# Optimization experiments

Measured on AMD Instinct MI355X. Metric: run time of the kernel, lower is better.

The kernel has to match this reference:

```python
import jax, jax.numpy as jnp
import numpy as np
import math

B, S, D, H = 2, 2048, 1024, 16
DK = D // H  # 64

def setup_inputs() -> dict:
    key = jax.random.key(0)
    ks = jax.random.split(key, 12)
    scale = 1.0 / math.sqrt(D)
    inp = {
        "query": jax.random.normal(ks[0], (B, S, D), jnp.float32),
        "key_": jax.random.normal(ks[1], (B, S, D), jnp.float32),
        "value": jax.random.normal(ks[2], (B, S, D), jnp.float32),
        "mask": jax.random.randint(ks[3], (B, 1, S, S), 0, 2, jnp.int32),
        "Wq": jax.random.normal(ks[4], (D, D), jnp.float32) * scale,
        "bq": jnp.zeros((D,), jnp.float32),
        "Wk": jax.random.normal(ks[5], (D, D), jnp.float32) * scale,
        "bk": jnp.zeros((D,), jnp.float32),
        "Wv": jax.random.normal(ks[6], (D, D), jnp.float32) * scale,
        "bv": jnp.zeros((D,), jnp.float32),
        "Wo": jax.random.normal(ks[7], (D, D), jnp.float32) * scale,
        "bo": jnp.zeros((D,), jnp.float32),
    }
    return inp

def _split_heads(x):  # [B,S,D] -> [B,H,S,DK]
    return x.reshape(B, -1, H, DK).transpose(0, 2, 1, 3)

def reference(query, key_, value, mask, Wq, bq, Wk, bk, Wv, bv, Wo, bo):
    # torch nn.Linear: y = x @ W^T + b
    q = _split_heads(query @ Wq.T + bq)
    k = _split_heads(key_ @ Wk.T + bk)
    v = _split_heads(value @ Wv.T + bv)
    scores = jnp.einsum("bhqd,bhkd->bhqk", q, k) / math.sqrt(DK)
    scores = jnp.where(mask == 0, jnp.float32(-1e9), scores)
    attn = jax.nn.softmax(scores, axis=-1)  # dropout is identity in eval mode
    ctx = jnp.einsum("bhqk,bhkd->bhqd", attn, v)
    ctx = ctx.transpose(0, 2, 1, 3).reshape(B, -1, D)
    return ctx @ Wo.T + bo
```

## Files before the change

kernel.cpp:

```cpp
#include <hip/hip_runtime.h>
#include <hip/hip_bf16.h>

typedef short s16x8 __attribute__((ext_vector_type(8)));
typedef float f32x4 __attribute__((ext_vector_type(4)));
typedef unsigned short u16;
typedef unsigned int u32;
typedef unsigned long long u64;

__device__ __forceinline__ u16 f2bf(float f) {
    union { float f; unsigned u; } c; c.f = f;
    unsigned u = c.u;
    return (u16)((u + 0x7fffu + ((u >> 16) & 1u)) >> 16);
}
__device__ __forceinline__ float bf2f(u32 lo16) {
    union { unsigned u; float f; } c; c.u = lo16 << 16; return c.f;
}
__device__ __forceinline__ u32 cvtpk(float lo, float hi) {
    u32 r;
    asm("v_cvt_pk_bf16_f32 %0, %1, %2" : "=v"(r) : "v"(lo), "v"(hi));
    return r;
}
__device__ __forceinline__ void gload16(const void* g, void* l) {
    __builtin_amdgcn_global_load_lds(
        (const __attribute__((address_space(1))) void*)g,
        (__attribute__((address_space(3))) void*)l, 16, 0, 0);
}

__global__ __launch_bounds__(256)
void conv_k(const float* __restrict__ q, const float* __restrict__ k, const float* __restrict__ v,
            const float* __restrict__ wq, const float* __restrict__ wk, const float* __restrict__ wv,
            const float* __restrict__ wo,
            u16* __restrict__ Qf, u16* __restrict__ Kf, u16* __restrict__ Vf,
            u16* __restrict__ Wqb, u16* __restrict__ Wkb, u16* __restrict__ Wvb, u16* __restrict__ Wob)
{
    const int gi = blockIdx.x * 256 + threadIdx.x;
    const float* src; u16* dst; int base;
    if (gi < 3 * 1048576) {
        const int seg = gi / 1048576;
        base = (gi - seg * 1048576) * 4;
        src = seg == 0 ? q : seg == 1 ? k : v;
        dst = seg == 0 ? Qf : seg == 1 ? Kf : Vf;
    } else {
        const int g2 = gi - 3 * 1048576;
        const int seg = g2 / 262144;
        base = (g2 - seg * 262144) * 4;
        src = seg == 0 ? wq : seg == 1 ? wk : seg == 2 ? wv : wo;
        dst = seg == 0 ? Wqb : seg == 1 ? Wkb : seg == 2 ? Wvb : Wob;
    }
    const float4 x = *(const float4*)(src + base);
    uint2 pk;
    pk.x = f2bf(x.x) | ((unsigned)f2bf(x.y) << 16);
    pk.y = f2bf(x.z) | ((unsigned)f2bf(x.w) << 16);
    *(uint2*)(dst + base) = pk;
}

__global__ __launch_bounds__(256)
void qkv_k(const u16* __restrict__ A0, const u16* __restrict__ A1, const u16* __restrict__ A2,
           const u16* __restrict__ W0, const u16* __restrict__ W1, const u16* __restrict__ W2,
           const float* __restrict__ b0, const float* __restrict__ b1, const float* __restrict__ b2,
           u16* __restrict__ O0, u16* __restrict__ O1, u16* __restrict__ O2)
{
    __shared__ u16 As[128 * 32];
    __shared__ u16 Bs[128 * 32];
    const int z = blockIdx.z;
    const u16* A = z == 0 ? A0 : z == 1 ? A1 : A2;
    const u16* W = z == 0 ? W0 : z == 1 ? W1 : W2;
    const float* bias = z == 0 ? b0 : z == 1 ? b1 : b2;
    u16* O = z == 0 ? O0 : z == 1 ? O1 : O2;

    const int tid = threadIdx.x, lane = tid & 63, wave = tid >> 6;
    const int wm = wave >> 1, wn = wave & 1;
    const int g = lane >> 4, q15 = lane & 15;
    const int m0 = blockIdx.x * 128, n0 = blockIdx.y * 128;
    const int lrow = lane >> 2, lcol = (lane & 3) * 8;

    f32x4 acc[4][4];
    #pragma unroll
    for (int i = 0; i < 4; i++)
        #pragma unroll
        for (int j = 0; j < 4; j++) acc[i][j] = f32x4{0.f, 0.f, 0.f, 0.f};

    for (int k0 = 0; k0 < 1024; k0 += 32) {
        __syncthreads();
        #pragma unroll
        for (int i = 0; i < 2; i++) {
            const int rr = i * 64 + wave * 16 + lrow;
            gload16(A + (size_t)(m0 + rr) * 1024 + k0 + lcol, &As[(i * 64 + wave * 16) * 32]);
            gload16(W + (size_t)(n0 + rr) * 1024 + k0 + lcol, &Bs[(i * 64 + wave * 16) * 32]);
        }
        __syncthreads();

        s16x8 af[4], bfr[4];
        #pragma unroll
        for (int mi = 0; mi < 4; mi++) af[mi]  = *(const s16x8*)&As[(wm * 64 + mi * 16 + q15) * 32 + g * 8];
        #pragma unroll
        for (int ni = 0; ni < 4; ni++) bfr[ni] = *(const s16x8*)&Bs[(wn * 64 + ni * 16 + q15) * 32 + g * 8];
        #pragma unroll
        for (int mi = 0; mi < 4; mi++)
            #pragma unroll
            for (int ni = 0; ni < 4; ni++)
                acc[mi][ni] = __builtin_amdgcn_mfma_f32_16x16x32_bf16(af[mi], bfr[ni], acc[mi][ni], 0, 0, 0);
    }

    #pragma unroll
    for (int mi = 0; mi < 4; mi++) {
        #pragma unroll
        for (int ni = 0; ni < 4; ni++) {
            const int n = n0 + wn * 64 + ni * 16 + q15;
            const float bn = bias[n];
            const int mbase = m0 + wm * 64 + mi * 16 + g * 4;
            if (z < 2) {
                #pragma unroll
                for (int r = 0; r < 4; r++)
                    O[(size_t)(mbase + r) * 1024 + n] = f2bf(acc[mi][ni][r] + bn);
            } else {
                const int bb = mbase >> 11;
                const int s  = mbase & 2047;
                const int h  = n >> 6, d = n & 63;
                u16 hv[4];
                #pragma unroll
                for (int r = 0; r < 4; r++) hv[r] = f2bf(acc[mi][ni][r] + bn);
                uint2 pk;
                pk.x = hv[0] | ((unsigned)hv[1] << 16);
                pk.y = hv[2] | ((unsigned)hv[3] << 16);
                *(uint2*)&O[(((size_t)(bb * 16 + h) * 64 + d) << 11) + s] = pk;
            }
        }
    }
}

__global__ __launch_bounds__(256)
void og_k(const u16* __restrict__ A, const u16* __restrict__ W,
          const float* __restrict__ bias, float* __restrict__ C)
{
    __shared__ u16 As[64 * 32];
    __shared__ u16 Bs[128 * 32];
    const int tid = threadIdx.x, lane = tid & 63, wave = tid >> 6;
    const int wm = wave >> 1, wn = wave & 1;
    const int g = lane >> 4, q15 = lane & 15;
    const int m0 = blockIdx.x * 64, n0 = blockIdx.y * 128;
    const int lrow = lane >> 2, lcol = (lane & 3) * 8;

    f32x4 acc[2][4];
    #pragma unroll
    for (int i = 0; i < 2; i++)
        #pragma unroll
        for (int j = 0; j < 4; j++) acc[i][j] = f32x4{0.f, 0.f, 0.f, 0.f};

    for (int k0 = 0; k0 < 1024; k0 += 32) {
        __syncthreads();
        {
            const int rr = wave * 16 + lrow;
            gload16(A + (size_t)(m0 + rr) * 1024 + k0 + lcol, &As[(wave * 16) * 32]);
        }
        #pragma unroll
        for (int i = 0; i < 2; i++) {
            const int rr = i * 64 + wave * 16 + lrow;
            gload16(W + (size_t)(n0 + rr) * 1024 + k0 + lcol, &Bs[(i * 64 + wave * 16) * 32]);
        }
        __syncthreads();

        s16x8 af[2], bfr[4];
        #pragma unroll
        for (int mi = 0; mi < 2; mi++) af[mi]  = *(const s16x8*)&As[(wm * 32 + mi * 16 + q15) * 32 + g * 8];
        #pragma unroll
        for (int ni = 0; ni < 4; ni++) bfr[ni] = *(const s16x8*)&Bs[(wn * 64 + ni * 16 + q15) * 32 + g * 8];
        #pragma unroll
        for (int mi = 0; mi < 2; mi++)
            #pragma unroll
            for (int ni = 0; ni < 4; ni++)
                acc[mi][ni] = __builtin_amdgcn_mfma_f32_16x16x32_bf16(af[mi], bfr[ni], acc[mi][ni], 0, 0, 0);
    }

    #pragma unroll
    for (int mi = 0; mi < 2; mi++) {
        #pragma unroll
        for (int ni = 0; ni < 4; ni++) {
            const int n = n0 + wn * 64 + ni * 16 + q15;
            const float bn = bias[n];
            const int mbase = m0 + wm * 32 + mi * 16 + g * 4;
            #pragma unroll
            for (int r = 0; r < 4; r++)
                C[(size_t)(mbase + r) * 1024 + n] = acc[mi][ni][r] + bn;
        }
    }
}

__global__ __launch_bounds__(256)
void pack_mask_k(const int* __restrict__ mask, u64* __restrict__ MB)
{
    const int wid  = blockIdx.x * 4 + (threadIdx.x >> 6);
    const int lane = threadIdx.x & 63;
    const int v = mask[(size_t)wid * 64 + lane];
    const u64 bits = __ballot(v != 0);
    if (lane == 0) MB[wid] = bits;
}

__global__ __launch_bounds__(256, 4)
void attn_k(const u16* __restrict__ Q, const u16* __restrict__ K,
            const u16* __restrict__ Vt, const u64* __restrict__ MB,
            u16* __restrict__ CtxP, float* __restrict__ LsumP)
{
    constexpr int S = 2048, D = 1024, DK = 64;
    __shared__ u16 Ks[64][72];
    __shared__ u16 Vs[64][72];
    __shared__ u16 Ps[4][32][72];
    const int tid = threadIdx.x, lane = tid & 63, wave = tid >> 6;
    const int g = lane >> 4, q15 = lane & 15;
    const int h = blockIdx.y;
    const int b = blockIdx.z >> 1, half = blockIdx.z & 1;
    const int qw = blockIdx.x * 128 + wave * 32;

    s16x8 qf[2][2];
    #pragma unroll
    for (int mf = 0; mf < 2; mf++)
        #pragma unroll
        for (int cc = 0; cc < 2; cc++)
            qf[mf][cc] = *(const s16x8*)(Q + ((size_t)b * S + qw + mf * 16 + q15) * D
                                           + h * DK + cc * 32 + g * 8);

    f32x4 accv[2][4];
    #pragma unroll
    for (int mf = 0; mf < 2; mf++)
        #pragma unroll
        for (int nf = 0; nf < 4; nf++)
            accv[mf][nf] = f32x4{0.f, 0.f, 0.f, 0.f};
    float lsum[2] = {0.f, 0.f};

    const size_t kgbase = (size_t)b * S * D + h * DK;
    const size_t vgbase = ((size_t)b * 16 + h) * DK * S;
    const size_t mbase  = ((size_t)b * S + qw + q15) * 32;

    for (int t = half * 16; t < half * 16 + 16; t++) {
        const int kv0 = t * 64;
        const u64 mw0 = MB[mbase + t];
        const u64 mw1 = MB[mbase + 512 + t];

        __syncthreads();
        #pragma unroll
        for (int i = 0; i < 2; i++) {
            const int c = tid + i * 256;
            const int row = c >> 3, col8 = (c & 7) * 8;
            *(s16x8*)&Ks[row][col8] = *(const s16x8*)(K + kgbase + (size_t)(kv0 + row) * D + col8);
            *(s16x8*)&Vs[row][col8] = *(const s16x8*)(Vt + vgbase + (size_t)row * S + kv0 + col8);
        }
        __syncthreads();

        f32x4 sc[2][4];
        #pragma unroll
        for (int nf = 0; nf < 4; nf++) {
            const s16x8 ka0 = *(const s16x8*)&Ks[nf * 16 + q15][g * 8];
            const s16x8 ka1 = *(const s16x8*)&Ks[nf * 16 + q15][32 + g * 8];
            #pragma unroll
            for (int mf = 0; mf < 2; mf++) {
                f32x4 s = f32x4{0.f, 0.f, 0.f, 0.f};
                s = __builtin_amdgcn_mfma_f32_16x16x32_bf16(ka0, qf[mf][0], s, 0, 0, 0);
                s = __builtin_amdgcn_mfma_f32_16x16x32_bf16(ka1, qf[mf][1], s, 0, 0, 0);
                sc[mf][nf] = s;
            }
        }

        #pragma unroll
        for (int mf = 0; mf < 2; mf++) {
            const u64 mw = mf ? mw1 : mw0;
            float part = 0.f;
            #pragma unroll
            for (int nf = 0; nf < 4; nf++) {
                const u32 nib = (u32)(mw >> (nf * 16 + g * 4)) & 0xFu;
                float p[4];
                #pragma unroll
                for (int r = 0; r < 4; r++) {
                    const float e = __expf(fmaf(sc[mf][nf][r], 0.125f, -8.0f));
                    p[r] = ((nib >> r) & 1u) ? e : 0.f;
                }
                part += (p[0] + p[1]) + (p[2] + p[3]);
                uint2 pk2;
                pk2.x = cvtpk(p[0], p[1]);
                pk2.y = cvtpk(p[2], p[3]);
                *(uint2*)&Ps[wave][mf * 16 + q15][nf * 16 + g * 4] = pk2;
            }
            lsum[mf] += part;
        }

        #pragma unroll
        for (int cc = 0; cc < 2; cc++) {
            s16x8 pa[2];
            #pragma unroll
            for (int mf = 0; mf < 2; mf++)
                pa[mf] = *(const s16x8*)&Ps[wave][mf * 16 + q15][cc * 32 + g * 8];
            #pragma unroll
            for (int nf = 0; nf < 4; nf++) {
                const s16x8 vb = *(const s16x8*)&Vs[nf * 16 + q15][cc * 32 + g * 8];
                #pragma unroll
                for (int mf = 0; mf < 2; mf++)
                    accv[mf][nf] = __builtin_amdgcn_mfma_f32_16x16x32_bf16(pa[mf], vb, accv[mf][nf], 0, 0, 0);
            }
        }
    }

    #pragma unroll
    for (int mf = 0; mf < 2; mf++) {
        float s_ = lsum[mf];
        s_ += __shfl_xor(s_, 16, 64);
        s_ += __shfl_xor(s_, 32, 64);
        lsum[mf] = s_;
    }
    const size_t pbase = (size_t)((half * 2 + b) * 16 + h) * S;
    if (lane < 16) {
        LsumP[pbase + qw + q15]      = lsum[0];
        LsumP[pbase + qw + 16 + q15] = lsum[1];
    }
    #pragma unroll
    for (int mf = 0; mf < 2; mf++)
        #pragma unroll
        for (int nf = 0; nf < 4; nf++)
            #pragma unroll
            for (int r = 0; r < 4; r++) {
                const int qrow = qw + mf * 16 + g * 4 + r;
                CtxP[(pbase + qrow) * 64 + nf * 16 + q15] = f2bf(accv[mf][nf][r]);
            }
}

__global__ __launch_bounds__(256)
void comb_k(const u16* __restrict__ CtxP, const float* __restrict__ LsumP,
            u16* __restrict__ Cx)
{
    const int gid = blockIdx.x * 256 + threadIdx.x;
    const int d4 = gid & 15;
    const int q  = (gid >> 4) & 2047;
    const int h  = (gid >> 15) & 15;
    const int bb = gid >> 19;
    const size_t i0 = ((size_t)(bb * 16 + h)) * 2048 + q;
    const size_t i1 = ((size_t)((2 + bb) * 16 + h)) * 2048 + q;
    const uint2 a = *(const uint2*)&CtxP[i0 * 64 + d4 * 4];
    const uint2 c = *(const uint2*)&CtxP[i1 * 64 + d4 * 4];
    const float rinv = __builtin_amdgcn_rcpf(LsumP[i0] + LsumP[i1]);
    const u32 au[2] = {a.x, a.y}, cu[2] = {c.x, c.y};
    uint2 o;
    u32 ow[2];
    #pragma unroll
    for (int j = 0; j < 2; j++) {
        const float lo = (bf2f(au[j] & 0xffffu) + bf2f(cu[j] & 0xffffu)) * rinv;
        const float hi = (bf2f(au[j] >> 16)     + bf2f(cu[j] >> 16))     * rinv;
        ow[j] = f2bf(lo) | ((u32)f2bf(hi) << 16);
    }
    o.x = ow[0]; o.y = ow[1];
    *(uint2*)&Cx[((size_t)bb * 2048 + q) * 1024 + h * 64 + d4 * 4] = o;
}

extern "C" void kernel_launch(void* const* d_in, const int* in_sizes, int n_in,
                              void* d_out, int out_size, void* d_ws, size_t ws_size,
                              hipStream_t stream)
{
    const float* query = (const float*)d_in[0];
    const float* key_  = (const float*)d_in[1];
    const float* value = (const float*)d_in[2];
    const int*   mask  = (const int*)d_in[3];
    const float* Wq = (const float*)d_in[4];
    const float* bq = (const float*)d_in[5];
    const float* Wk = (const float*)d_in[6];
    const float* bk = (const float*)d_in[7];
    const float* Wv = (const float*)d_in[8];
    const float* bv = (const float*)d_in[9];
    const float* Wo = (const float*)d_in[10];
    const float* bo = (const float*)d_in[11];

    char* ws = (char*)d_ws;
    u16* Qf   = (u16*)(ws);
    u16* Kf   = (u16*)(ws + (size_t)( 8 << 20));
    u16* Vf   = (u16*)(ws + (size_t)(16 << 20));
    u16* Wqb  = (u16*)(ws + (size_t)(24 << 20));
    u16* Wkb  = (u16*)(ws + (size_t)(26 << 20));
    u16* Wvb  = (u16*)(ws + (size_t)(28 << 20));
    u16* Wob  = (u16*)(ws + (size_t)(30 << 20));
    u16* Qb   = (u16*)(ws + (size_t)(32 << 20));
    u16* Kb   = (u16*)(ws + (size_t)(40 << 20));
    u16* Vt   = (u16*)(ws + (size_t)(48 << 20));
    u64* MBp  = (u64*)(ws + (size_t)(56 << 20));
    float* LsP = (float*)(ws + (size_t)(57 << 20));
    u16* CtxP = Qf;
    u16* Cx   = Qb;

    dim3 bb2(256, 1, 1);
    conv_k<<<dim3(16384, 1, 1), bb2, 0, stream>>>(query, key_, value, Wq, Wk, Wv, Wo,
                                                  Qf, Kf, Vf, Wqb, Wkb, Wvb, Wob);
    qkv_k<<<dim3(32, 8, 3), bb2, 0, stream>>>(Qf, Kf, Vf, Wqb, Wkb, Wvb,
                                              bq, bk, bv, Qb, Kb, Vt);
    pack_mask_k<<<dim3(32768, 1, 1), bb2, 0, stream>>>(mask, MBp);
    attn_k<<<dim3(16, 16, 4), bb2, 0, stream>>>(Qb, Kb, Vt, MBp, CtxP, LsP);
    comb_k<<<dim3(4096, 1, 1), bb2, 0, stream>>>(CtxP, LsP, Cx);
    og_k<<<dim3(64, 8, 1), bb2, 0, stream>>>(Cx, Wob, bo, (float*)d_out);
}
```

Before: 173.7 us.

## Rewrite attention kernel with 32x32 MFMA, register-resident P, and double-buffered async staging

Reworks the attention inner loop to use 32x32x16 bf16 MFMAs. The S^T layout lets the exponentiated probabilities feed the PV MFMA straight from registers, which removes the per-wave LDS round trip for P. K/V tiles are staged with global_load_lds into XOR-swizzled double buffers, so the next tile's load overlaps compute, with explicit vmcnt waits and barriers. The exp is switched to exp2 with a folded scale, and setprio hints are added around the MFMA blocks. This increases register pressure and adds complex swizzle indexing that must match the MFMA operand layouts.

```diff
diff --git a/kernel.cpp b/kernel.cpp
--- a/kernel.cpp
+++ b/kernel.cpp
@@ -2,7 +2,9 @@
 #include <hip/hip_bf16.h>
 
 typedef short s16x8 __attribute__((ext_vector_type(8)));
+typedef short s16x4 __attribute__((ext_vector_type(4)));
 typedef float f32x4 __attribute__((ext_vector_type(4)));
+typedef float f32x16 __attribute__((ext_vector_type(16)));
 typedef unsigned short u16;
 typedef unsigned int u32;
 typedef unsigned long long u64;
@@ -116,14 +118,14 @@
             } else {
                 const int bb = mbase >> 11;
                 const int s  = mbase & 2047;
-                const int h  = n >> 6, d = n & 63;
+                const int hd = n >> 6, d = n & 63;
                 u16 hv[4];
                 #pragma unroll
                 for (int r = 0; r < 4; r++) hv[r] = f2bf(acc[mi][ni][r] + bn);
                 uint2 pk;
                 pk.x = hv[0] | ((unsigned)hv[1] << 16);
                 pk.y = hv[2] | ((unsigned)hv[3] << 16);
-                *(uint2*)&O[(((size_t)(bb * 16 + h) * 64 + d) << 11) + s] = pk;
+                *(uint2*)&O[(((size_t)(bb * 16 + hd) * 64 + d) << 11) + s] = pk;
             }
         }
     }
@@ -201,124 +203,124 @@
             const u16* __restrict__ Vt, const u64* __restrict__ MB,
             u16* __restrict__ CtxP, float* __restrict__ LsumP)
 {
-    constexpr int S = 2048, D = 1024, DK = 64;
-    __shared__ u16 Ks[64][72];
-    __shared__ u16 Vs[64][72];
-    __shared__ u16 Ps[4][32][72];
+    constexpr int S = 2048;
+    __shared__ u16 Ks[2][64][64];
+    __shared__ u16 Vs[2][64][64];
     const int tid = threadIdx.x, lane = tid & 63, wave = tid >> 6;
-    const int g = lane >> 4, q15 = lane & 15;
-    const int h = blockIdx.y;
+    const int l31 = lane & 31, h = lane >> 5, x7 = lane & 7;
+    const int hh = blockIdx.y;
     const int b = blockIdx.z >> 1, half = blockIdx.z & 1;
     const int qw = blockIdx.x * 128 + wave * 32;
-
-    s16x8 qf[2][2];
-    #pragma unroll
-    for (int mf = 0; mf < 2; mf++)
-        #pragma unroll
-        for (int cc = 0; cc < 2; cc++)
-            qf[mf][cc] = *(const s16x8*)(Q + ((size_t)b * S + qw + mf * 16 + q15) * D
-                                           + h * DK + cc * 32 + g * 8);
-
-    f32x4 accv[2][4];
-    #pragma unroll
-    for (int mf = 0; mf < 2; mf++)
-        #pragma unroll
-        for (int nf = 0; nf < 4; nf++)
-            accv[mf][nf] = f32x4{0.f, 0.f, 0.f, 0.f};
-    float lsum[2] = {0.f, 0.f};
-
-    const size_t kgbase = (size_t)b * S * D + h * DK;
-    const size_t vgbase = ((size_t)b * 16 + h) * DK * S;
-    const size_t mbase  = ((size_t)b * S + qw + q15) * 32;
-
-    for (int t = half * 16; t < half * 16 + 16; t++) {
-        const int kv0 = t * 64;
-        const u64 mw0 = MB[mbase + t];
-        const u64 mw1 = MB[mbase + 512 + t];
-
-        __syncthreads();
+    const int t0 = half * 16;
+
+    const size_t kgbase = (size_t)b * S * 1024 + hh * 64;
+    const size_t vgbase = (size_t)(b * 16 + hh) * 64 * 2048;
+
+    s16x8 qf[4];
+    #pragma unroll
+    for (int s = 0; s < 4; s++)
+        qf[s] = *(const s16x8*)(Q + ((size_t)b * S + qw + l31) * 1024 + hh * 64 + s * 16 + h * 8);
+
+    f32x16 acc[2];
+    #pragma unroll
+    for (int r = 0; r < 16; r++) { acc[0][r] = 0.f; acc[1][r] = 0.f; }
+    float lsum = 0.f;
+
+    const int srl = lane >> 3;
+    const int scs = ((lane & 7) ^ srl) * 8;
+    auto STAGE = [&](int buf, int kv0) {
         #pragma unroll
         for (int i = 0; i < 2; i++) {
-            const int c = tid + i * 256;
-            const int row = c >> 3, col8 = (c & 7) * 8;
-            *(s16x8*)&Ks[row][col8] = *(const s16x8*)(K + kgbase + (size_t)(kv0 + row) * D + col8);
-            *(s16x8*)&Vs[row][col8] = *(const s16x8*)(Vt + vgbase + (size_t)row * S + kv0 + col8);
-        }
-        __syncthreads();
-
-        f32x4 sc[2][4];
-        #pragma unroll
-        for (int nf = 0; nf < 4; nf++) {
-            const s16x8 ka0 = *(const s16x8*)&Ks[nf * 16 + q15][g * 8];
-            const s16x8 ka1 = *(const s16x8*)&Ks[nf * 16 + q15][32 + g * 8];
-            #pragma unroll
-            for (int mf = 0; mf < 2; mf++) {
-                f32x4 s = f32x4{0.f, 0.f, 0.f, 0.f};
-                s = __builtin_amdgcn_mfma_f32_16x16x32_bf16(ka0, qf[mf][0], s, 0, 0, 0);
-                s = __builtin_amdgcn_mfma_f32_16x16x32_bf16(ka1, qf[mf][1], s, 0, 0, 0);
-                sc[mf][nf] = s;
+            const int rb = i * 32 + wave * 8;
+            gload16(K + kgbase + (size_t)(kv0 + rb + srl) * 1024 + scs, &Ks[buf][rb][0]);
+            gload16(Vt + vgbase + (size_t)(rb + srl) * 2048 + kv0 + scs, &Vs[buf][rb][0]);
+        }
+    };
+
+    const u64* mwp = MB + ((size_t)b * S + qw + l31) * 32 + t0;
+    STAGE(0, t0 * 64);
+
+    for (int t = 0; t < 16; t++) {
+        const int buf = t & 1;
+        const u64 mw = mwp[t];
+        if (t < 15) {
+            STAGE(buf ^ 1, (t0 + t + 1) * 64);
+            asm volatile("s_waitcnt vmcnt(4)" ::: "memory");
+        } else {
+            asm volatile("s_waitcnt vmcnt(0)" ::: "memory");
+        }
+        __builtin_amdgcn_s_barrier();
+        __builtin_amdgcn_sched_barrier(0);
+
+        f32x16 sc[2];
+        #pragma unroll
+        for (int r = 0; r < 16; r++) { sc[0][r] = 0.f; sc[1][r] = 0.f; }
+        __builtin_amdgcn_s_setprio(1);
+        #pragma unroll
+        for (int s = 0; s < 4; s++) {
+            const int ce = (((s << 1) | h) ^ x7) << 3;
+            const s16x8 ka0 = *(const s16x8*)&Ks[buf][l31][ce];
+            const s16x8 ka1 = *(const s16x8*)&Ks[buf][32 + l31][ce];
+            sc[0] = __builtin_amdgcn_mfma_f32_32x32x16_bf16(ka0, qf[s], sc[0], 0, 0, 0);
+            sc[1] = __builtin_amdgcn_mfma_f32_32x32x16_bf16(ka1, qf[s], sc[1], 0, 0, 0);
+        }
+        __builtin_amdgcn_s_setprio(0);
+
+        s16x8 pa[4];
+        #pragma unroll
+        for (int kvb = 0; kvb < 2; kvb++) {
+            const u32 mh = ((u32)(mw >> (kvb * 32))) >> (h * 4);
+            float p[16];
+            #pragma unroll
+            for (int r = 0; r < 16; r++) {
+                const int bit = (r & 3) + ((r >> 2) << 3);
+                const float e = __builtin_amdgcn_exp2f(fmaf(sc[kvb][r], 0.18033688f, -11.5415603f));
+                p[r] = ((mh >> bit) & 1u) ? e : 0.f;
             }
-        }
-
-        #pragma unroll
-        for (int mf = 0; mf < 2; mf++) {
-            const u64 mw = mf ? mw1 : mw0;
-            float part = 0.f;
-            #pragma unroll
-            for (int nf = 0; nf < 4; nf++) {
-                const u32 nib = (u32)(mw >> (nf * 16 + g * 4)) & 0xFu;
-                float p[4];
-                #pragma unroll
-                for (int r = 0; r < 4; r++) {
-                    const float e = __expf(fmaf(sc[mf][nf][r], 0.125f, -8.0f));
-                    p[r] = ((nib >> r) & 1u) ? e : 0.f;
-                }
-                part += (p[0] + p[1]) + (p[2] + p[3]);
-                uint2 pk2;
-                pk2.x = cvtpk(p[0], p[1]);
-                pk2.y = cvtpk(p[2], p[3]);
-                *(uint2*)&Ps[wave][mf * 16 + q15][nf * 16 + g * 4] = pk2;
+            lsum += (((p[0] + p[1]) + (p[2] + p[3])) + ((p[4] + p[5]) + (p[6] + p[7])))
+                  + (((p[8] + p[9]) + (p[10] + p[11])) + ((p[12] + p[13]) + (p[14] + p[15])));
+            #pragma unroll
+            for (int sub = 0; sub < 2; sub++) {
+                const int base = sub * 8;
+                union { u32 w[4]; s16x8 v; } u;
+                u.w[0] = cvtpk(p[base + 0], p[base + 1]);
+                u.w[1] = cvtpk(p[base + 2], p[base + 3]);
+                u.w[2] = cvtpk(p[base + 4], p[base + 5]);
+                u.w[3] = cvtpk(p[base + 6], p[base + 7]);
+                pa[kvb * 2 + sub] = u.v;
             }
-            lsum[mf] += part;
-        }
-
-        #pragma unroll
-        for (int cc = 0; cc < 2; cc++) {
-            s16x8 pa[2];
-            #pragma unroll
-            for (int mf = 0; mf < 2; mf++)
-                pa[mf] = *(const s16x8*)&Ps[wave][mf * 16 + q15][cc * 32 + g * 8];
-            #pragma unroll
-            for (int nf = 0; nf < 4; nf++) {
-                const s16x8 vb = *(const s16x8*)&Vs[nf * 16 + q15][cc * 32 + g * 8];
-                #pragma unroll
-                for (int mf = 0; mf < 2; mf++)
-                    accv[mf][nf] = __builtin_amdgcn_mfma_f32_16x16x32_bf16(pa[mf], vb, accv[mf][nf], 0, 0, 0);
-            }
-        }
-    }
-
-    #pragma unroll
-    for (int mf = 0; mf < 2; mf++) {
-        float s_ = lsum[mf];
-        s_ += __shfl_xor(s_, 16, 64);
-        s_ += __shfl_xor(s_, 32, 64);
-        lsum[mf] = s_;
-    }
-    const size_t pbase = (size_t)((half * 2 + b) * 16 + h) * S;
-    if (lane < 16) {
-        LsumP[pbase + qw + q15]      = lsum[0];
-        LsumP[pbase + qw + 16 + q15] = lsum[1];
-    }
-    #pragma unroll
-    for (int mf = 0; mf < 2; mf++)
-        #pragma unroll
-        for (int nf = 0; nf < 4; nf++)
-            #pragma unroll
-            for (int r = 0; r < 4; r++) {
-                const int qrow = qw + mf * 16 + g * 4 + r;
-                CtxP[(pbase + qrow) * 64 + nf * 16 + q15] = f2bf(accv[mf][nf][r]);
-            }
+        }
+
+        __builtin_amdgcn_s_setprio(1);
+        #pragma unroll
+        for (int s = 0; s < 4; s++) {
+            const int e0 = (((2 * s)     ^ x7) << 3) + 4 * h;
+            const int e1 = (((2 * s + 1) ^ x7) << 3) + 4 * h;
+            union { s16x4 q2[2]; s16x8 v; } u0, u1;
+            u0.q2[0] = *(const s16x4*)&Vs[buf][l31][e0];
+            u0.q2[1] = *(const s16x4*)&Vs[buf][l31][e1];
+            u1.q2[0] = *(const s16x4*)&Vs[buf][32 + l31][e0];
+            u1.q2[1] = *(const s16x4*)&Vs[buf][32 + l31][e1];
+            acc[0] = __builtin_amdgcn_mfma_f32_32x32x16_bf16(pa[s], u0.v, acc[0], 0, 0, 0);
+            acc[1] = __builtin_amdgcn_mfma_f32_32x32x16_bf16(pa[s], u1.v, acc[1], 0, 0, 0);
+        }
+        __builtin_amdgcn_s_setprio(0);
+        __builtin_amdgcn_s_barrier();
+    }
+
+    lsum += __shfl_xor(lsum, 32, 64);
+    const size_t pbase = (size_t)((half * 2 + b) * 16 + hh) * S;
+    if (lane < 32) LsumP[pbase + qw + l31] = lsum;
+
+    #pragma unroll
+    for (int db = 0; db < 2; db++)
+        #pragma unroll
+        for (int r = 0; r < 16; r += 2) {
+            const int q1 = qw + (r & 3) + ((r >> 2) << 3) + h * 4;
+            const u32 w = cvtpk(acc[db][r], acc[db][r + 1]);
+            CtxP[(pbase + q1) * 64 + db * 32 + l31]     = (u16)(w & 0xffffu);
+            CtxP[(pbase + q1 + 1) * 64 + db * 32 + l31] = (u16)(w >> 16);
+        }
 }
 
 __global__ __launch_bounds__(256)
@@ -328,10 +330,10 @@
     const int gid = blockIdx.x * 256 + threadIdx.x;
     const int d4 = gid & 15;
     const int q  = (gid >> 4) & 2047;
-    const int h  = (gid >> 15) & 15;
+    const int hd = (gid >> 15) & 15;
     const int bb = gid >> 19;
-    const size_t i0 = ((size_t)(bb * 16 + h)) * 2048 + q;
-    const size_t i1 = ((size_t)((2 + bb) * 16 + h)) * 2048 + q;
+    const size_t i0 = ((size_t)(bb * 16 + hd)) * 2048 + q;
+    const size_t i1 = ((size_t)((2 + bb) * 16 + hd)) * 2048 + q;
     const uint2 a = *(const uint2*)&CtxP[i0 * 64 + d4 * 4];
     const uint2 c = *(const uint2*)&CtxP[i1 * 64 + d4 * 4];
     const float rinv = __builtin_amdgcn_rcpf(LsumP[i0] + LsumP[i1]);
@@ -345,7 +347,7 @@
         ow[j] = f2bf(lo) | ((u32)f2bf(hi) << 16);
     }
     o.x = ow[0]; o.y = ow[1];
-    *(uint2*)&Cx[((size_t)bb * 2048 + q) * 1024 + h * 64 + d4 * 4] = o;
+    *(uint2*)&Cx[((size_t)bb * 2048 + q) * 1024 + hd * 64 + d4 * 4] = o;
 }
 
 extern "C" void kernel_launch(void* const* d_in, const int* in_sizes, int n_in,
```

New measurement: 161.7 us. 1.07x faster.
